# Kernel optimization log

Hardware: AMD Instinct MI355X
Metric: run time of the kernel (lower is better)

## Reference

```python
import jax, jax.numpy as jnp
import numpy as np

C_S, C_Z, C_ATOM, H, RBF = 128, 64, 16, 4, 16
N_RES, E_RES, N_ATOM, E_ATOM = 1000, 4000, 14000, 784000


def _p(key, shape, scale=0.05):
    return (jax.random.normal(key, shape, dtype=jnp.float32) * scale)


def setup_inputs() -> dict:
    key = jax.random.key(0)
    ks = jax.random.split(key, 24)
    inp = {
        "node_features": jax.random.normal(ks[0], (N_RES, C_S), dtype=jnp.float32),
        "res_edge_features": jax.random.normal(ks[1], (E_RES, C_Z), dtype=jnp.float32),
        "res_edge_index": jax.random.randint(ks[2], (2, E_RES), 0, N_RES),
        "atom_features": jax.random.normal(ks[3], (N_ATOM, C_ATOM), dtype=jnp.float32),
        "atom_coords": jax.random.normal(ks[4], (N_ATOM, 3), dtype=jnp.float32),
        "cross_atom_edge_index": jax.random.randint(ks[5], (2, E_ATOM), 0, N_ATOM),
        "atom_edge_to_res_edge": jax.random.randint(ks[6], (E_ATOM,), 0, E_RES),
        # atom_dist_embed MLP: RBF -> RBF -> RBF -> H
        "rbf_w1": _p(ks[7], (RBF, RBF)), "rbf_b1": jnp.zeros((RBF,), jnp.float32),
        "rbf_w2": _p(ks[8], (RBF, RBF)), "rbf_b2": jnp.zeros((RBF,), jnp.float32),
        "rbf_w3": _p(ks[9], (RBF, H)),  "rbf_b3": jnp.zeros((H,), jnp.float32),
        # res_level_bias MLP: (2*c_s + c_z) -> c_atom -> H
        "rb_w1": _p(ks[10], (2 * C_S + C_Z, C_ATOM)), "rb_b1": jnp.zeros((C_ATOM,), jnp.float32),
        "rb_w2": _p(ks[11], (C_ATOM, H)), "rb_b2": jnp.zeros((H,), jnp.float32),
        # q / kv / out projections
        "wq": _p(ks[12], (C_ATOM, C_ATOM * H)),     "bq": jnp.zeros((C_ATOM * H,), jnp.float32),
        "wkv": _p(ks[13], (C_ATOM, 2 * C_ATOM * H)), "bkv": jnp.zeros((2 * C_ATOM * H,), jnp.float32),
        "wo": _p(ks[14], (C_ATOM * H, C_ATOM)),     "bo": jnp.zeros((C_ATOM,), jnp.float32),
    }
    return inp


def _rbf(d, d_min=0.0, d_max=20.0, d_count=RBF):
    mu = jnp.linspace(d_min, d_max, d_count, dtype=jnp.float32)
    sigma = (d_max - d_min) / d_count
    return jnp.exp(-(((d[..., None] - mu) / sigma) ** 2))


def _seg_softmax(x, idx, n_seg):
    # scatter-softmax over segments (pyg_utils.softmax), per head column
    m = jax.ops.segment_max(x, idx, num_segments=n_seg)
    e = jnp.exp(x - m[idx])
    s = jax.ops.segment_sum(e, idx, num_segments=n_seg)
    return e / (s[idx] + 1e-16)


def reference(node_features, res_edge_features, res_edge_index, atom_features,
              atom_coords, cross_atom_edge_index, atom_edge_to_res_edge,
              rbf_w1, rbf_b1, rbf_w2, rbf_b2, rbf_w3, rbf_b3,
              rb_w1, rb_b1, rb_w2, rb_b2, wq, bq, wkv, bkv, wo, bo,
              eps=1e-8):
    src = cross_atom_edge_index[1]
    dst = cross_atom_edge_index[0]

    # RBF distance bias  [E_atom, H]
    vec = atom_coords[dst] - atom_coords[src]
    d = jnp.linalg.norm(vec + eps, axis=-1)
    h = jax.nn.relu(_rbf(d) @ rbf_w1 + rbf_b1)
    h = jax.nn.relu(h @ rbf_w2 + rbf_b2)
    atom_dist_bias = h @ rbf_w3 + rbf_b3

    # residue-level bias  [E_res, H]
    cat = jnp.concatenate([res_edge_features,
                           node_features[res_edge_index[0]],
                           node_features[res_edge_index[1]]], axis=-1)
    res_level_bias = jax.nn.relu(cat @ rb_w1 + rb_b1) @ rb_w2 + rb_b2

    # gathered q / k / v  [E_atom, H, c_atom]
    q = (atom_features @ wq + bq)[src].reshape(-1, H, C_ATOM)
    kv = (atom_features @ wkv + bkv)[dst].reshape(-1, H, 2 * C_ATOM)
    k, v = kv[..., :C_ATOM], kv[..., C_ATOM:]

    R = jnp.einsum('ehc,ehc->eh', q, k) / np.sqrt(C_ATOM)
    R = R + res_level_bias[atom_edge_to_res_edge] + atom_dist_bias

    # atom-level scatter-softmax over edges grouped by src atom
    alpha = _seg_softmax(R, src, N_ATOM)

    # residue-level: scatter-mean of scores per residue edge, then softmax by dst res
    cnt = jax.ops.segment_sum(jnp.ones((R.shape[0],), R.dtype),
                              atom_edge_to_res_edge, num_segments=E_RES)
    block_r = jax.ops.segment_sum(R, atom_edge_to_res_edge, num_segments=E_RES)
    block_r = block_r / jnp.clip(cnt, 1.0)[:, None]
    beta = _seg_softmax(block_r, res_edge_index[1], N_RES)

    w = alpha * beta[atom_edge_to_res_edge]           # [E_atom, H]
    atom_update = jax.ops.segment_sum(w[..., None] * v, src, num_segments=N_ATOM)
    return atom_update.reshape(-1, H * C_ATOM) @ wo + bo
```

## Files before the change

kernel.cpp:

```cpp
#include <hip/hip_runtime.h>

#define NH 4
#define N_RES 1000
#define E_RES 4000
#define N_ATOM 14000
#define E_ATOM 784000
#define MAXS 128
#define NBRE 256
#define TABN 16385
#define TINV 512.0f

#define BUILD_BLKS ((E_ATOM + 255) / 256)
#define PROJ_BLKS ((N_ATOM * 192 + 255) / 256)
#define RLB_BLKS (E_RES / 4)
#define TAB_BLKS ((TABN + 255) / 256)

typedef float f32x4 __attribute__((ext_vector_type(4)));

__device__ __forceinline__ unsigned enc_f(float f) {
  unsigned u = __float_as_uint(f);
  return (u & 0x80000000u) ? ~u : (u | 0x80000000u);
}
__device__ __forceinline__ float dec_f(unsigned e) {
  unsigned u = (e & 0x80000000u) ? (e & 0x7FFFFFFFu) : ~e;
  return __uint_as_float(u);
}

__global__ __launch_bounds__(256) void kA(
    const int* __restrict__ cei, const int* __restrict__ aer,
    int* __restrict__ cnt_src, unsigned* __restrict__ pay,
    const float* __restrict__ af, const float* __restrict__ wq,
    const float* __restrict__ bq, const float* __restrict__ wkv,
    const float* __restrict__ bkv, float* __restrict__ Qa,
    float* __restrict__ Ka, float* __restrict__ Va,
    const float* __restrict__ ref_, const float* __restrict__ nf,
    const int* __restrict__ rei, const float* __restrict__ w1,
    const float* __restrict__ b1, const float* __restrict__ w2,
    const float* __restrict__ b2, float* __restrict__ rlb,
    const float* __restrict__ rw1, const float* __restrict__ rb1,
    const float* __restrict__ rw2, const float* __restrict__ rb2,
    const float* __restrict__ rw3, const float* __restrict__ rb3,
    f32x4* __restrict__ tab) {
  int b = blockIdx.x;
  if (b < BUILD_BLKS) {
    int e = b * 256 + threadIdx.x;
    if (e < E_ATOM) {
      int src = cei[E_ATOM + e];
      int dst = cei[e];
      int re = aer[e];
      int slot = atomicAdd(&cnt_src[src], 1);
      if (slot >= MAXS) slot = MAXS - 1;
      pay[(size_t)src * MAXS + slot] = (unsigned)dst | ((unsigned)re << 16);
    }
  } else if (b < BUILD_BLKS + PROJ_BLKS) {
    int tid = (b - BUILD_BLKS) * 256 + threadIdx.x;
    if (tid < N_ATOM * 192) {
      int a = tid / 192, j = tid % 192;
      const float* row = af + a * 16;
      if (j < 64) {
        float acc = bq[j];
#pragma unroll
        for (int i = 0; i < 16; ++i) acc += row[i] * wq[i * 64 + j];
        Qa[a * 64 + j] = acc;
      } else if (j < 128) {
        int jj = j - 64;
        int col = ((jj >> 4) << 5) + (jj & 15);
        float acc = bkv[col];
#pragma unroll
        for (int i = 0; i < 16; ++i) acc += row[i] * wkv[i * 128 + col];
        Ka[a * 64 + jj] = acc;
      } else {
        int jj = j - 128;
        int col = ((jj >> 4) << 5) + 16 + (jj & 15);
        float acc = bkv[col];
#pragma unroll
        for (int i = 0; i < 16; ++i) acc += row[i] * wkv[i * 128 + col];
        Va[a * 64 + jj] = acc;
      }
    }
  } else if (b < BUILD_BLKS + PROJ_BLKS + RLB_BLKS) {
    __shared__ float hid[4][16];
    int sub = threadIdx.x >> 6, l = threadIdx.x & 63;
    int r = (b - BUILD_BLKS - PROJ_BLKS) * 4 + sub;
    int r0 = rei[r], r1 = rei[E_RES + r];
    int j = l >> 2, pq = l & 3;
    float acc = 0.f;
    for (int i = pq; i < 320; i += 4) {
      float cc;
      if (i < 64) cc = ref_[r * 64 + i];
      else if (i < 192) cc = nf[r0 * 128 + (i - 64)];
      else cc = nf[r1 * 128 + (i - 192)];
      acc += cc * w1[i * 16 + j];
    }
    acc += __shfl_xor(acc, 1);
    acc += __shfl_xor(acc, 2);
    if (pq == 0) hid[sub][j] = fmaxf(acc + b1[j], 0.f);
    __syncthreads();
    if (l < 4) {
      float o = b2[l];
#pragma unroll
      for (int jj = 0; jj < 16; ++jj) o += hid[sub][jj] * w2[jj * 4 + l];
      rlb[r * 4 + l] = o;
    }
  } else {
    int i = (b - BUILD_BLKS - PROJ_BLKS - RLB_BLKS) * 256 + threadIdx.x;
    if (i < TABN) {
      float d = (float)i * (1.0f / TINV);
      float rb[16], h1[16], h2[16];
      const float step = 20.0f / 15.0f;
      const float inv_sigma = 1.0f / 1.25f;
#pragma unroll
      for (int jj = 0; jj < 16; ++jj) {
        float t = (d - jj * step) * inv_sigma;
        rb[jj] = __expf(-t * t);
      }
#pragma unroll
      for (int k = 0; k < 16; ++k) {
        float acc = rb1[k];
#pragma unroll
        for (int jj = 0; jj < 16; ++jj) acc += rb[jj] * rw1[jj * 16 + k];
        h1[k] = fmaxf(acc, 0.f);
      }
#pragma unroll
      for (int k = 0; k < 16; ++k) {
        float acc = rb2[k];
#pragma unroll
        for (int jj = 0; jj < 16; ++jj) acc += h1[jj] * rw2[jj * 16 + k];
        h2[k] = fmaxf(acc, 0.f);
      }
      f32x4 o;
#pragma unroll
      for (int h = 0; h < NH; ++h) {
        float acc = rb3[h];
#pragma unroll
        for (int jj = 0; jj < 16; ++jj) acc += h2[jj] * rw3[jj * 4 + h];
        o[h] = acc;
      }
      tab[i] = o;
    }
  }
}

__global__ __launch_bounds__(256) void k_edgeR(
    const int* __restrict__ cnt_src, const unsigned* __restrict__ pay,
    const float* __restrict__ coords, const float* __restrict__ Qa,
    const float* __restrict__ Ka, const float* __restrict__ rlb,
    const f32x4* __restrict__ tab, float* __restrict__ R_slab) {
  int l = threadIdx.x;
  int a = blockIdx.x * 2 + (l >> 7);
  int s = l & 127;
  int n = cnt_src[a];
  if (n > MAXS) n = MAXS;
  if (s >= n) return;
  unsigned pr = pay[(size_t)a * MAXS + s];
  int dst = (int)(pr & 0xFFFFu);
  int re = (int)(pr >> 16);
  float vx = coords[dst * 3 + 0] - coords[a * 3 + 0] + 1e-8f;
  float vy = coords[dst * 3 + 1] - coords[a * 3 + 1] + 1e-8f;
  float vz = coords[dst * 3 + 2] - coords[a * 3 + 2] + 1e-8f;
  float d = sqrtf(vx * vx + vy * vy + vz * vz);
  float x = d * TINV;
  int i = (int)x;
  if (i > TABN - 2) i = TABN - 2;
  float fr = x - (float)i;
  f32x4 t0 = tab[i], t1 = tab[i + 1];
  f32x4 adb = t0 + (t1 - t0) * fr;
  const float4* qp = (const float4*)(Qa + (size_t)a * 64);
  const float4* kp = (const float4*)(Ka + (size_t)dst * 64);
  float4 rlb4 = *(const float4*)(rlb + re * 4);
  const float* rlbp = (const float*)&rlb4;
  f32x4 Rv;
#pragma unroll
  for (int h = 0; h < NH; ++h) {
    float dot = 0.f;
#pragma unroll
    for (int v4 = 0; v4 < 4; ++v4) {
      float4 q4 = qp[h * 4 + v4];
      float4 k4 = kp[h * 4 + v4];
      dot += q4.x * k4.x + q4.y * k4.y + q4.z * k4.z + q4.w * k4.w;
    }
    Rv[h] = dot * 0.25f + rlbp[h] + adb[h];
  }
  __builtin_nontemporal_store(Rv,
                              (f32x4*)(R_slab + (size_t)(a * MAXS + s) * 4));
}

__global__ __launch_bounds__(1024) void k_re2(
    const int* __restrict__ cnt_src, const unsigned* __restrict__ pay,
    const float* __restrict__ R_slab, int* __restrict__ cntg,
    float* __restrict__ br_g) {
  __shared__ __align__(16) unsigned char smraw[64000];
  int* scnt = (int*)smraw;
  float* sbr = (float*)smraw;
  int tid = threadIdx.x;
  int bid = blockIdx.x;
  int wv = tid >> 6, lane = tid & 63;
  int gw = bid * 16 + wv;
  for (int j = tid; j < E_RES; j += 1024) scnt[j] = 0;
  __syncthreads();
  for (int a = gw; a < N_ATOM; a += NBRE * 16) {
    int n = cnt_src[a];
    if (n > MAXS) n = MAXS;
    size_t base = (size_t)a * MAXS;
    for (int i = lane; i < n; i += 64) {
      int re = (int)(pay[base + i] >> 16);
      atomicAdd(&scnt[re], 1);
    }
  }
  __syncthreads();
  for (int j = tid; j < E_RES; j += 1024) cntg[bid * E_RES + j] = scnt[j];
  __syncthreads();
  for (int j = tid; j < E_RES * 4; j += 1024) sbr[j] = 0.f;
  __syncthreads();
  for (int a = gw; a < N_ATOM; a += NBRE * 16) {
    int n = cnt_src[a];
    if (n > MAXS) n = MAXS;
    size_t base = (size_t)a * MAXS;
    for (int i = lane; i < n; i += 64) {
      int re = (int)(pay[base + i] >> 16);
      f32x4 r = *(const f32x4*)(R_slab + (base + i) * 4);
      atomicAdd(&sbr[re * 4 + 0], r[0]);
      atomicAdd(&sbr[re * 4 + 1], r[1]);
      atomicAdd(&sbr[re * 4 + 2], r[2]);
      atomicAdd(&sbr[re * 4 + 3], r[3]);
    }
  }
  __syncthreads();
  for (int j = tid; j < E_RES * 4; j += 1024)
    br_g[(size_t)bid * E_RES * 4 + j] = sbr[j];
}

__global__ __launch_bounds__(256) void k_red(const float* __restrict__ br_g,
                                             const int* __restrict__ cntg,
                                             float* __restrict__ block_r) {
  int t = blockIdx.x * blockDim.x + threadIdx.x;
  if (t >= E_RES * 4) return;
  int r = t >> 2;
  float s = 0.f;
  int c = 0;
  for (int b = 0; b < NBRE; ++b) {
    s += br_g[(size_t)b * E_RES * 4 + t];
    c += cntg[b * E_RES + r];
  }
  block_r[t] = s / fmaxf((float)c, 1.0f);
}

__global__ __launch_bounds__(1024) void k_br23(
    const float* __restrict__ block_r, const int* __restrict__ rei,
    float* __restrict__ beta) {
  __shared__ unsigned resm[N_RES * 4];
  __shared__ float ress[N_RES * 4];
  int tid = threadIdx.x;
  for (int j = tid; j < N_RES * 4; j += 1024) { resm[j] = 0u; ress[j] = 0.f; }
  __syncthreads();
  float brv[4][4];
  int r1v[4];
  for (int k = 0; k < 4; ++k) {
    int r = tid + k * 1024;
    if (r < E_RES) {
      r1v[k] = rei[E_RES + r];
#pragma unroll
      for (int h = 0; h < 4; ++h) {
        brv[k][h] = block_r[r * 4 + h];
        atomicMax(&resm[r1v[k] * 4 + h], enc_f(brv[k][h]));
      }
    }
  }
  __syncthreads();
  for (int k = 0; k < 4; ++k) {
    int r = tid + k * 1024;
    if (r < E_RES) {
#pragma unroll
      for (int h = 0; h < 4; ++h)
        atomicAdd(&ress[r1v[k] * 4 + h],
                  __expf(brv[k][h] - dec_f(resm[r1v[k] * 4 + h])));
    }
  }
  __syncthreads();
  for (int k = 0; k < 4; ++k) {
    int r = tid + k * 1024;
    if (r < E_RES) {
#pragma unroll
      for (int h = 0; h < 4; ++h)
        beta[r * 4 + h] = __expf(brv[k][h] - dec_f(resm[r1v[k] * 4 + h])) /
                          (ress[r1v[k] * 4 + h] + 1e-16f);
    }
  }
}

__global__ __launch_bounds__(256) void k_src(
    const int* __restrict__ cnt_src, const unsigned* __restrict__ pay,
    const float* __restrict__ R_slab, const float* __restrict__ beta,
    const float* __restrict__ Va, float* __restrict__ au) {
  int wid = (blockIdx.x * blockDim.x + threadIdx.x) >> 6;
  int l = threadIdx.x & 63;
  if (wid >= N_ATOM) return;
  int n = cnt_src[wid];
  if (n > MAXS) n = MAXS;
  int h = l >> 4;
  size_t rbase = (size_t)wid * MAXS;
  float m0 = -3.0e38f, m1 = -3.0e38f, m2 = -3.0e38f, m3 = -3.0e38f;
  for (int i = l; i < n; i += 64) {
    f32x4 r = *(const f32x4*)(R_slab + (rbase + i) * 4);
    m0 = fmaxf(m0, r[0]); m1 = fmaxf(m1, r[1]);
    m2 = fmaxf(m2, r[2]); m3 = fmaxf(m3, r[3]);
  }
#pragma unroll
  for (int off = 1; off < 64; off <<= 1) {
    m0 = fmaxf(m0, __shfl_xor(m0, off));
    m1 = fmaxf(m1, __shfl_xor(m1, off));
    m2 = fmaxf(m2, __shfl_xor(m2, off));
    m3 = fmaxf(m3, __shfl_xor(m3, off));
  }
  float mh = (h < 2) ? ((h == 0) ? m0 : m1) : ((h == 2) ? m2 : m3);
  float s = 0.f, acc = 0.f;
#pragma unroll 2
  for (int i = 0; i < n; ++i) {
    unsigned pr = pay[rbase + i];
    int dst = (int)(pr & 0xFFFFu);
    int re = (int)(pr >> 16);
    float rv = R_slab[(rbase + i) * 4 + h];
    float bt = beta[re * 4 + h];
    float v = Va[(size_t)dst * 64 + l];
    float pw = __expf(rv - mh);
    s += pw;
    acc += pw * bt * v;
  }
  au[(size_t)wid * 64 + l] = acc / (s + 1e-16f);
}

__global__ __launch_bounds__(256) void k_out(
    const float* __restrict__ au, const float* __restrict__ wo,
    const float* __restrict__ bo, float* __restrict__ out) {
  int t = blockIdx.x * blockDim.x + threadIdx.x;
  if (t >= N_ATOM * 16) return;
  int a = t >> 4, c = t & 15;
  float acc = bo[c];
  const float* r = au + (size_t)a * 64;
#pragma unroll
  for (int j = 0; j < 64; ++j) acc += r[j] * wo[j * 16 + c];
  out[t] = acc;
}

extern "C" void kernel_launch(void* const* d_in, const int* in_sizes, int n_in,
                              void* d_out, int out_size, void* d_ws,
                              size_t ws_size, hipStream_t stream) {
  const float* nf   = (const float*)d_in[0];
  const float* ref_ = (const float*)d_in[1];
  const int*   rei  = (const int*)d_in[2];
  const float* af   = (const float*)d_in[3];
  const float* co   = (const float*)d_in[4];
  const int*   cei  = (const int*)d_in[5];
  const int*   aer  = (const int*)d_in[6];
  const float* rw1  = (const float*)d_in[7];
  const float* rb1  = (const float*)d_in[8];
  const float* rw2  = (const float*)d_in[9];
  const float* rb2  = (const float*)d_in[10];
  const float* rw3  = (const float*)d_in[11];
  const float* rb3  = (const float*)d_in[12];
  const float* w1   = (const float*)d_in[13];
  const float* b1   = (const float*)d_in[14];
  const float* w2   = (const float*)d_in[15];
  const float* b2   = (const float*)d_in[16];
  const float* wq   = (const float*)d_in[17];
  const float* bq   = (const float*)d_in[18];
  const float* wkv  = (const float*)d_in[19];
  const float* bkv  = (const float*)d_in[20];
  const float* wo   = (const float*)d_in[21];
  const float* bo   = (const float*)d_in[22];
  float* out = (float*)d_out;

  float* ws = (float*)d_ws;
  float*    Qa      = ws;
  float*    Ka      = Qa + 896000;
  float*    Va      = Ka + 896000;
  float*    rlb     = Va + 896000;
  float*    R_slab  = rlb + 16000;
  unsigned* pay     = (unsigned*)(R_slab + 7168000);
  float*    br_g    = (float*)(pay + 1792000);
  int*      cntg    = (int*)(br_g + 4096000);
  int*      cnt_src = cntg + 1024000;
  float*    block_r = (float*)(cnt_src + 14000);
  f32x4*    tab     = (f32x4*)(block_r + 16000);
  float*    au      = Qa;
  float*    beta    = Ka + 16000;

  hipMemsetAsync((void*)cnt_src, 0, 14000 * 4, stream);

  kA<<<BUILD_BLKS + PROJ_BLKS + RLB_BLKS + TAB_BLKS, 256, 0, stream>>>(
      cei, aer, cnt_src, pay, af, wq, bq, wkv, bkv, Qa, Ka, Va, ref_, nf, rei,
      w1, b1, w2, b2, rlb, rw1, rb1, rw2, rb2, rw3, rb3, tab);
  k_edgeR<<<N_ATOM / 2, 256, 0, stream>>>(cnt_src, pay, co, Qa, Ka, rlb, tab,
                                          R_slab);
  k_re2<<<NBRE, 1024, 0, stream>>>(cnt_src, pay, R_slab, cntg, br_g);
  k_red<<<(E_RES * 4 + 255) / 256, 256, 0, stream>>>(br_g, cntg, block_r);
  k_br23<<<1, 1024, 0, stream>>>(block_r, rei, beta);
  k_src<<<(N_ATOM * 64 + 255) / 256, 256, 0, stream>>>(cnt_src, pay, R_slab,
                                                       beta, Va, au);
  k_out<<<(N_ATOM * 16 + 255) / 256, 256, 0, stream>>>(au, wo, bo, out);
}
```

Measured before the change: 258.4 us.

## Fuse atom softmax stats into edge-score kernel and output projection into aggregation

After: 252.4 us. 1.02x faster.

```diff
diff --git a/kernel.cpp b/kernel.cpp
--- a/kernel.cpp
+++ b/kernel.cpp
@@ -145,44 +145,76 @@
     const int* __restrict__ cnt_src, const unsigned* __restrict__ pay,
     const float* __restrict__ coords, const float* __restrict__ Qa,
     const float* __restrict__ Ka, const float* __restrict__ rlb,
-    const f32x4* __restrict__ tab, float* __restrict__ R_slab) {
-  int l = threadIdx.x;
-  int a = blockIdx.x * 2 + (l >> 7);
-  int s = l & 127;
+    const f32x4* __restrict__ tab, float* __restrict__ R_slab,
+    f32x4* __restrict__ msm, f32x4* __restrict__ mss) {
+  int l = threadIdx.x & 63;
+  int a = blockIdx.x * 4 + (threadIdx.x >> 6);
   int n = cnt_src[a];
   if (n > MAXS) n = MAXS;
-  if (s >= n) return;
-  unsigned pr = pay[(size_t)a * MAXS + s];
-  int dst = (int)(pr & 0xFFFFu);
-  int re = (int)(pr >> 16);
-  float vx = coords[dst * 3 + 0] - coords[a * 3 + 0] + 1e-8f;
-  float vy = coords[dst * 3 + 1] - coords[a * 3 + 1] + 1e-8f;
-  float vz = coords[dst * 3 + 2] - coords[a * 3 + 2] + 1e-8f;
-  float d = sqrtf(vx * vx + vy * vy + vz * vz);
-  float x = d * TINV;
-  int i = (int)x;
-  if (i > TABN - 2) i = TABN - 2;
-  float fr = x - (float)i;
-  f32x4 t0 = tab[i], t1 = tab[i + 1];
-  f32x4 adb = t0 + (t1 - t0) * fr;
+  size_t base = (size_t)a * MAXS;
+  float ax = coords[a * 3 + 0], ay = coords[a * 3 + 1], az = coords[a * 3 + 2];
   const float4* qp = (const float4*)(Qa + (size_t)a * 64);
-  const float4* kp = (const float4*)(Ka + (size_t)dst * 64);
-  float4 rlb4 = *(const float4*)(rlb + re * 4);
-  const float* rlbp = (const float*)&rlb4;
-  f32x4 Rv;
-#pragma unroll
-  for (int h = 0; h < NH; ++h) {
-    float dot = 0.f;
-#pragma unroll
-    for (int v4 = 0; v4 < 4; ++v4) {
-      float4 q4 = qp[h * 4 + v4];
-      float4 k4 = kp[h * 4 + v4];
-      dot += q4.x * k4.x + q4.y * k4.y + q4.z * k4.z + q4.w * k4.w;
-    }
-    Rv[h] = dot * 0.25f + rlbp[h] + adb[h];
-  }
-  __builtin_nontemporal_store(Rv,
-                              (f32x4*)(R_slab + (size_t)(a * MAXS + s) * 4));
+  bool a0 = l < n, a1 = l + 64 < n;
+  f32x4 R0, R1;
+#pragma unroll
+  for (int sl = 0; sl < 2; ++sl) {
+    bool act = sl ? a1 : a0;
+    f32x4 Rv = {-3.0e38f, -3.0e38f, -3.0e38f, -3.0e38f};
+    if (act) {
+      int s = l + sl * 64;
+      unsigned pr = pay[base + s];
+      int dst = (int)(pr & 0xFFFFu);
+      int re = (int)(pr >> 16);
+      float vx = coords[dst * 3 + 0] - ax + 1e-8f;
+      float vy = coords[dst * 3 + 1] - ay + 1e-8f;
+      float vz = coords[dst * 3 + 2] - az + 1e-8f;
+      float d = sqrtf(vx * vx + vy * vy + vz * vz);
+      float x = d * TINV;
+      int i = (int)x;
+      if (i > TABN - 2) i = TABN - 2;
+      float fr = x - (float)i;
+      f32x4 t0 = tab[i], t1 = tab[i + 1];
+      f32x4 adb = t0 + (t1 - t0) * fr;
+      const float4* kp = (const float4*)(Ka + (size_t)dst * 64);
+      float4 rlb4 = *(const float4*)(rlb + re * 4);
+      const float* rlbp = (const float*)&rlb4;
+#pragma unroll
+      for (int h = 0; h < NH; ++h) {
+        float dot = 0.f;
+#pragma unroll
+        for (int v4 = 0; v4 < 4; ++v4) {
+          float4 q4 = qp[h * 4 + v4];
+          float4 k4 = kp[h * 4 + v4];
+          dot += q4.x * k4.x + q4.y * k4.y + q4.z * k4.z + q4.w * k4.w;
+        }
+        Rv[h] = dot * 0.25f + rlbp[h] + adb[h];
+      }
+      __builtin_nontemporal_store(Rv, (f32x4*)(R_slab + (base + s) * 4));
+    }
+    if (sl) R1 = Rv; else R0 = Rv;
+  }
+  f32x4 mx;
+#pragma unroll
+  for (int h = 0; h < NH; ++h) mx[h] = fmaxf(R0[h], R1[h]);
+#pragma unroll
+  for (int off = 1; off < 64; off <<= 1) {
+#pragma unroll
+    for (int h = 0; h < NH; ++h) mx[h] = fmaxf(mx[h], __shfl_xor(mx[h], off));
+  }
+  f32x4 ex;
+#pragma unroll
+  for (int h = 0; h < NH; ++h)
+    ex[h] = (a0 ? __expf(R0[h] - mx[h]) : 0.f) +
+            (a1 ? __expf(R1[h] - mx[h]) : 0.f);
+#pragma unroll
+  for (int off = 1; off < 64; off <<= 1) {
+#pragma unroll
+    for (int h = 0; h < NH; ++h) ex[h] += __shfl_xor(ex[h], off);
+  }
+  if (l == 0) {
+    msm[a] = mx;
+    mss[a] = ex;
+  }
 }
 
 __global__ __launch_bounds__(1024) void k_re2(
@@ -291,29 +323,20 @@
 __global__ __launch_bounds__(256) void k_src(
     const int* __restrict__ cnt_src, const unsigned* __restrict__ pay,
     const float* __restrict__ R_slab, const float* __restrict__ beta,
-    const float* __restrict__ Va, float* __restrict__ au) {
-  int wid = (blockIdx.x * blockDim.x + threadIdx.x) >> 6;
-  int l = threadIdx.x & 63;
-  if (wid >= N_ATOM) return;
+    const float* __restrict__ Va, const f32x4* __restrict__ msm,
+    const f32x4* __restrict__ mss, const float* __restrict__ wo,
+    const float* __restrict__ bo, float* __restrict__ out) {
+  __shared__ float sau[4][64];
+  int wv = threadIdx.x >> 6, l = threadIdx.x & 63;
+  int wid = blockIdx.x * 4 + wv;
   int n = cnt_src[wid];
   if (n > MAXS) n = MAXS;
   int h = l >> 4;
   size_t rbase = (size_t)wid * MAXS;
-  float m0 = -3.0e38f, m1 = -3.0e38f, m2 = -3.0e38f, m3 = -3.0e38f;
-  for (int i = l; i < n; i += 64) {
-    f32x4 r = *(const f32x4*)(R_slab + (rbase + i) * 4);
-    m0 = fmaxf(m0, r[0]); m1 = fmaxf(m1, r[1]);
-    m2 = fmaxf(m2, r[2]); m3 = fmaxf(m3, r[3]);
-  }
-#pragma unroll
-  for (int off = 1; off < 64; off <<= 1) {
-    m0 = fmaxf(m0, __shfl_xor(m0, off));
-    m1 = fmaxf(m1, __shfl_xor(m1, off));
-    m2 = fmaxf(m2, __shfl_xor(m2, off));
-    m3 = fmaxf(m3, __shfl_xor(m3, off));
-  }
-  float mh = (h < 2) ? ((h == 0) ? m0 : m1) : ((h == 2) ? m2 : m3);
-  float s = 0.f, acc = 0.f;
+  f32x4 m4 = msm[wid], s4 = mss[wid];
+  float mh = m4[h];
+  float sden = s4[h] + 1e-16f;
+  float acc = 0.f;
 #pragma unroll 2
   for (int i = 0; i < n; ++i) {
     unsigned pr = pay[rbase + i];
@@ -322,24 +345,18 @@
     float rv = R_slab[(rbase + i) * 4 + h];
     float bt = beta[re * 4 + h];
     float v = Va[(size_t)dst * 64 + l];
-    float pw = __expf(rv - mh);
-    s += pw;
-    acc += pw * bt * v;
-  }
-  au[(size_t)wid * 64 + l] = acc / (s + 1e-16f);
-}
-
-__global__ __launch_bounds__(256) void k_out(
-    const float* __restrict__ au, const float* __restrict__ wo,
-    const float* __restrict__ bo, float* __restrict__ out) {
-  int t = blockIdx.x * blockDim.x + threadIdx.x;
-  if (t >= N_ATOM * 16) return;
-  int a = t >> 4, c = t & 15;
-  float acc = bo[c];
-  const float* r = au + (size_t)a * 64;
-#pragma unroll
-  for (int j = 0; j < 64; ++j) acc += r[j] * wo[j * 16 + c];
-  out[t] = acc;
+    acc += __expf(rv - mh) * bt * v;
+  }
+  sau[wv][l] = acc / sden;
+  __syncthreads();
+  int p = l >> 4, c = l & 15;
+  float part = 0.f;
+#pragma unroll
+  for (int jj = 0; jj < 16; ++jj)
+    part += sau[wv][p * 16 + jj] * wo[(p * 16 + jj) * 16 + c];
+  part += __shfl_down(part, 32);
+  part += __shfl_down(part, 16);
+  if (l < 16) out[wid * 16 + c] = part + bo[c];
 }
 
 extern "C" void kernel_launch(void* const* d_in, const int* in_sizes, int n_in,
@@ -382,7 +399,8 @@
   int*      cnt_src = cntg + 1024000;
   float*    block_r = (float*)(cnt_src + 14000);
   f32x4*    tab     = (f32x4*)(block_r + 16000);
-  float*    au      = Qa;
+  f32x4*    msm     = (f32x4*)((float*)tab + 65544);
+  f32x4*    mss     = (f32x4*)((float*)msm + 56000);
   float*    beta    = Ka + 16000;
 
   hipMemsetAsync((void*)cnt_src, 0, 14000 * 4, stream);
@@ -390,12 +408,11 @@
   kA<<<BUILD_BLKS + PROJ_BLKS + RLB_BLKS + TAB_BLKS, 256, 0, stream>>>(
       cei, aer, cnt_src, pay, af, wq, bq, wkv, bkv, Qa, Ka, Va, ref_, nf, rei,
       w1, b1, w2, b2, rlb, rw1, rb1, rw2, rb2, rw3, rb3, tab);
-  k_edgeR<<<N_ATOM / 2, 256, 0, stream>>>(cnt_src, pay, co, Qa, Ka, rlb, tab,
-                                          R_slab);
+  k_edgeR<<<N_ATOM / 4, 256, 0, stream>>>(cnt_src, pay, co, Qa, Ka, rlb, tab,
+                                          R_slab, msm, mss);
   k_re2<<<NBRE, 1024, 0, stream>>>(cnt_src, pay, R_slab, cntg, br_g);
   k_red<<<(E_RES * 4 + 255) / 256, 256, 0, stream>>>(br_g, cntg, block_r);
   k_br23<<<1, 1024, 0, stream>>>(block_r, rei, beta);
-  k_src<<<(N_ATOM * 64 + 255) / 256, 256, 0, stream>>>(cnt_src, pay, R_slab,
-                                                       beta, Va, au);
-  k_out<<<(N_ATOM * 16 + 255) / 256, 256, 0, stream>>>(au, wo, bo, out);
-}
+  k_src<<<N_ATOM / 4, 256, 0, stream>>>(cnt_src, pay, R_slab, beta, Va, msm,
+                                        mss, wo, bo, out);
+}
```
